# Kernel tuning notes

Hardware: AMD Instinct MI355X
Metric: run time of the kernel (lower is better)

Reference implementation:

```python
import jax, jax.numpy as jnp
import numpy as np

N, E, R = 50000, 500000, 3
IN, HID, OUT = 128, 128, 128
NEG_SLOPE = 0.2


def setup_inputs() -> dict:
    key = jax.random.key(0)
    ks = jax.random.split(key, 16)
    g = lambda i, shape: jax.random.normal(ks[i], shape, jnp.float32) * 0.1
    return {
        "x": jax.random.normal(ks[0], (N, IN), jnp.float32),
        "edge_index": jax.random.randint(ks[1], (2, E), 0, N, jnp.int32),
        "edge_type": jax.random.randint(ks[2], (E,), 0, R, jnp.int32),
        "edge_attr": jax.random.normal(ks[3], (E, 1), jnp.float32),
        # conv1 params (RGATConv: per-relation weight, q/k/e attention vectors, edge lin, bias)
        "w1": g(4, (R, IN, HID)), "q1": g(5, (HID, 1)), "k1": g(6, (HID, 1)),
        "le1": g(7, (1, HID)), "e1": g(8, (HID, 1)), "b1": jnp.zeros((HID,), jnp.float32),
        # conv2 params
        "w2": g(9, (R, HID, OUT)), "q2": g(10, (OUT, 1)), "k2": g(11, (OUT, 1)),
        "le2": g(12, (1, OUT)), "e2": g(13, (OUT, 1)), "b2": jnp.zeros((OUT,), jnp.float32),
    }


def _rgat_conv(x, src, dst, edge_type, edge_attr, w, q, k, le, e, b):
    """PyG RGATConv: heads=1, dim=1, additive-self-attention, across-relation softmax."""
    n = x.shape[0]
    # Per-relation linear at node level (equiv. to per-edge bmm with w[edge_type])
    xw = jnp.einsum('ni,rio->rno', x, w)            # [R, N, C]
    x_j = xw[edge_type, src]                          # [E, C] transformed source feats
    x_i = xw[edge_type, dst]                          # [E, C] transformed target feats
    # additive attention logits: q(x_i) + k(x_j) + e(lin_edge(edge_attr))
    alpha = x_i @ q + x_j @ k + (edge_attr @ le) @ e  # [E, 1]
    alpha = jax.nn.leaky_relu(alpha, negative_slope=NEG_SLOPE)
    # across-relation softmax over incoming edges of each target node
    amax = jax.ops.segment_max(alpha, dst, num_segments=n)
    amax = jnp.where(jnp.isfinite(amax), amax, 0.0)   # empty segments -> 0
    ex = jnp.exp(alpha - amax[dst])
    denom = jax.ops.segment_sum(ex, dst, num_segments=n)
    alpha = ex / (denom[dst] + 1e-16)
    # weighted scatter-add aggregation, then bias (concat=True, heads=1)
    out = jax.ops.segment_sum(alpha * x_j, dst, num_segments=n)  # [N, C]
    return out + b


def reference(x, edge_index, edge_type, edge_attr,
              w1, q1, k1, le1, e1, b1,
              w2, q2, k2, le2, e2, b2):
    src, dst = edge_index[0], edge_index[1]
    h = jax.nn.relu(_rgat_conv(x, src, dst, edge_type, edge_attr, w1, q1, k1, le1, e1, b1))
    return _rgat_conv(h, src, dst, edge_type, edge_attr, w2, q2, k2, le2, e2, b2)
```

## Files before the change

### kernel.cpp

```cpp
#include <hip/hip_runtime.h>
#include <hip/hip_bf16.h>
#include <math.h>

typedef __bf16 bf16x8 __attribute__((ext_vector_type(8)));
typedef float f32x4 __attribute__((ext_vector_type(4)));

#define CDIM 128

__global__ void sentinel_kernel(float* outf) {
  if (threadIdx.x == 0) outf[0] = 12345.0f;
}

__global__ __launch_bounds__(256) void prep_kernel(
    const float* __restrict__ w1, const float* __restrict__ w2,
    __hip_bfloat16* __restrict__ wt,
    const float* __restrict__ le1, const float* __restrict__ e1,
    const float* __restrict__ le2, const float* __restrict__ e2,
    float* __restrict__ outc, int* __restrict__ deg, int perW, int n) {
  const int b = blockIdx.x;
  const int tid = threadIdx.x;
  if (b < 48) {
    int t = b * 256 + tid;
    if (t >= perW * 2) return;
    const float* w = (t < perW) ? w1 : w2;
    int tt = (t < perW) ? t : t - perW;
    int r = tt >> 11;
    int rem = tt & 2047;
    int kb = rem >> 7;
    int o = rem & 127;
    const float* wr = w + ((size_t)r << 14);
    union { __hip_bfloat16 h[8]; int4 v; } u;
#pragma unroll
    for (int j = 0; j < 8; ++j)
      u.h[j] = __float2bfloat16(wr[(size_t)(kb * 8 + j) * CDIM + o]);
    *reinterpret_cast<int4*>(wt + (size_t)t * 8) = u.v;
  } else if (b == 48) {
    if (tid < 64) {
      float v1 = le1[tid] * e1[tid] + le1[tid + 64] * e1[tid + 64];
      float v2 = le2[tid] * e2[tid] + le2[tid + 64] * e2[tid + 64];
#pragma unroll
      for (int off = 32; off > 0; off >>= 1) {
        v1 += __shfl_xor(v1, off, 64);
        v2 += __shfl_xor(v2, off, 64);
      }
      if (tid == 0) { outc[0] = v1; outc[1] = v2; }
    }
  } else {
    int i = (b - 49) * 256 + tid;
    if (i < n) deg[i] = 0;
  }
}


__global__ __launch_bounds__(256) void hist_kernel(const int* __restrict__ dstv,
                                                   int* __restrict__ deg, int E) {
  int e = blockIdx.x * 256 + threadIdx.x;
  if (e < E) atomicAdd(&deg[dstv[e]], 1);
}

__global__ __launch_bounds__(256) void scan1_kernel(const int* __restrict__ deg,
                                                    int* __restrict__ rowptr,
                                                    int* __restrict__ partials, int n) {
  __shared__ int sh[256];
  int t = threadIdx.x;
  int base = blockIdx.x * 1024;
  int idx = base + t * 4;
  int v[4]; int s = 0;
#pragma unroll
  for (int j = 0; j < 4; ++j) { v[j] = (idx + j < n) ? deg[idx + j] : 0; s += v[j]; }
  sh[t] = s;
  __syncthreads();
  for (int off = 1; off < 256; off <<= 1) {
    int x = (t >= off) ? sh[t - off] : 0;
    __syncthreads();
    sh[t] += x;
    __syncthreads();
  }
  int excl = sh[t] - s;
  if (t == 255) partials[blockIdx.x] = sh[255];
  int run = excl;
#pragma unroll
  for (int j = 0; j < 4; ++j) {
    if (idx + j < n) rowptr[idx + j] = run;
    run += v[j];
  }
}

__global__ __launch_bounds__(256) void scan3_kernel(int* __restrict__ rowptr,
                                                    int* __restrict__ cursor,
                                                    const int* __restrict__ partials,
                                                    int nb, int n, int E) {
  __shared__ int spfx[64];
  int t = threadIdx.x;
  if (t < 64) {
    int pv = (t < nb) ? partials[t] : 0;
    int v = pv;
#pragma unroll
    for (int off = 1; off < 64; off <<= 1) {
      int u = __shfl_up(v, off, 64);
      if (t >= off) v += u;
    }
    spfx[t] = v - pv;
  }
  __syncthreads();
  int i = blockIdx.x * 256 + t;
  if (i < n) {
    int v = rowptr[i] + spfx[i >> 10];
    rowptr[i] = v;
    cursor[i] = v;
  } else if (i == n) {
    rowptr[n] = E;
  }
}

__global__ __launch_bounds__(256) void scatter_kernel(
    const int* __restrict__ srcv, const int* __restrict__ dstv,
    const int* __restrict__ etype, const float* __restrict__ eattr,
    int* __restrict__ cursor, int2* __restrict__ kattr, int E, int n) {
  int e = blockIdx.x * 256 + threadIdx.x;
  if (e >= E) return;
  int p = atomicAdd(&cursor[dstv[e]], 1);
  kattr[p] = make_int2(etype[e] * n + srcv[e], __float_as_int(eattr[e]));
}

__global__ __launch_bounds__(256) void gemm_xw_kernel(
    const float* __restrict__ xin, const __hip_bfloat16* __restrict__ wt,
    const float* __restrict__ qv, const float* __restrict__ kv,
    __hip_bfloat16* __restrict__ xwout, float* __restrict__ sq, float* __restrict__ sk,
    int n) {
  __shared__ __hip_bfloat16 wlds[16 * 128 * 8];
  __shared__ float qls[128], kls[128];
  const int base = blockIdx.x * 64;
  const int tid = threadIdx.x;
  const int wave = tid >> 6, lane = tid & 63;
  const int quad = lane >> 4, c16 = lane & 15;

  if (tid < 128) qls[tid] = qv[tid];
  else kls[tid - 128] = kv[tid - 128];

  bf16x8 zf;
#pragma unroll
  for (int j = 0; j < 8; ++j) zf[j] = (__bf16)0.0f;

  const int m = base + wave * 16 + c16;
  const bool ok = m < n;
  bf16x8 af[4];
#pragma unroll
  for (int ks = 0; ks < 4; ++ks) {
    if (ok) {
      const float* xp = xin + (size_t)m * CDIM + ks * 32 + quad * 8;
      f32x4 x0 = *reinterpret_cast<const f32x4*>(xp);
      f32x4 x1 = *reinterpret_cast<const f32x4*>(xp + 4);
      bf16x8 a;
#pragma unroll
      for (int j = 0; j < 4; ++j) { a[j] = (__bf16)x0[j]; a[4 + j] = (__bf16)x1[j]; }
      af[ks] = a;
    } else {
      af[ks] = zf;
    }
  }

  for (int r = 0; r < 3; ++r) {
    if (r) __syncthreads();
    {
      const int4* src = reinterpret_cast<const int4*>(wt + ((size_t)r << 14));
      int4* dst = reinterpret_cast<int4*>(wlds);
#pragma unroll
      for (int i = 0; i < 8; ++i) dst[tid + i * 256] = src[tid + i * 256];
    }
    __syncthreads();

    f32x4 acc[8];
#pragma unroll
    for (int ot = 0; ot < 8; ++ot) acc[ot] = (f32x4){0.f, 0.f, 0.f, 0.f};

#pragma unroll
    for (int ks = 0; ks < 4; ++ks) {
#pragma unroll
      for (int ot = 0; ot < 8; ++ot) {
        bf16x8 b = *reinterpret_cast<const bf16x8*>(
            &wlds[(((ks * 4 + quad) * 128) + ot * 16 + c16) * 8]);
        acc[ot] = __builtin_amdgcn_mfma_f32_16x16x32_bf16(b, af[ks], acc[ot], 0, 0, 0);
      }
    }

    __hip_bfloat16* rp = xwout + (((size_t)r * n + m) << 7) + quad * 4;
    float s_q = 0.f, s_k = 0.f;
#pragma unroll
    for (int ot = 0; ot < 8; ++ot) {
      f32x4 a = acc[ot];
      f32x4 q4 = *reinterpret_cast<const f32x4*>(&qls[ot * 16 + quad * 4]);
      f32x4 k4 = *reinterpret_cast<const f32x4*>(&kls[ot * 16 + quad * 4]);
      s_q += a[0] * q4[0] + a[1] * q4[1] + a[2] * q4[2] + a[3] * q4[3];
      s_k += a[0] * k4[0] + a[1] * k4[1] + a[2] * k4[2] + a[3] * k4[3];
      if (ok) {
        union { __hip_bfloat16 b4[4]; uint2 u; } pk;
#pragma unroll
        for (int t = 0; t < 4; ++t) pk.b4[t] = __float2bfloat16(a[t]);
        *reinterpret_cast<uint2*>(rp + ot * 16) = pk.u;
      }
    }
    s_q += __shfl_xor(s_q, 16, 64);
    s_q += __shfl_xor(s_q, 32, 64);
    s_k += __shfl_xor(s_k, 16, 64);
    s_k += __shfl_xor(s_k, 32, 64);
    if (quad == 0 && ok) {
      sq[(size_t)r * n + m] = s_q;
      sk[(size_t)r * n + m] = s_k;
    }
  }
}

__global__ __launch_bounds__(256) void aggregate_kernel(
    const int* __restrict__ rowptr, const int2* __restrict__ kattr,
    const float* __restrict__ sq, const float* __restrict__ sk,
    const __hip_bfloat16* __restrict__ xw, const float* __restrict__ bias,
    const float* __restrict__ cscal, float* __restrict__ out, int n, int do_relu) {
  const int wave = threadIdx.x >> 6, lane = threadIdx.x & 63;
  const int node = blockIdx.x * 4 + wave;
  if (node >= n) return;
  const int g = lane >> 4;
  const int sub = lane & 15;
  const float c = cscal[0];
  const int n2 = n * 2;

  const int start = rowptr[node];
  const int deg = rowptr[node + 1] - start;
  const float s0 = sq[node], s1 = sq[n + node], s2 = sq[n2 + node];

  float acc[8];
#pragma unroll
  for (int t = 0; t < 8; ++t) acc[t] = 0.f;
  float den = 0.f;

  for (int j0 = 0; j0 < deg; j0 += 16) {
    const int jb = j0 + (g << 2);
    int2 ka[4];
#pragma unroll
    for (int t = 0; t < 4; ++t) {
      int idx = jb + t;
      ka[t] = kattr[start + (idx < deg ? idx : 0)];
    }
    float w[4];
    bf16x8 f[4];
#pragma unroll
    for (int t = 0; t < 4; ++t) {
      int kk = ka[t].x;
      float sv = (kk >= n2) ? s2 : ((kk >= n) ? s1 : s0);
      float l = sv + sk[kk] + c * __int_as_float(ka[t].y);
      l = l > 0.f ? l : 0.2f * l;
      w[t] = (jb + t < deg) ? __expf(l) : 0.f;
      f[t] = *reinterpret_cast<const bf16x8*>(xw + ((size_t)kk << 7) + sub * 8);
    }
#pragma unroll
    for (int t = 0; t < 8; ++t)
      acc[t] += w[0] * (float)f[0][t] + w[1] * (float)f[1][t] +
                w[2] * (float)f[2][t] + w[3] * (float)f[3][t];
    den += (w[0] + w[1]) + (w[2] + w[3]);
  }

#pragma unroll
  for (int t = 0; t < 8; ++t) {
    acc[t] += __shfl_xor(acc[t], 16, 64);
    acc[t] += __shfl_xor(acc[t], 32, 64);
  }
  den += __shfl_xor(den, 16, 64);
  den += __shfl_xor(den, 32, 64);

  if (g == 0) {
    float inv = 1.0f / (den + 1e-16f);
    f32x4 b0 = *reinterpret_cast<const f32x4*>(bias + sub * 8);
    f32x4 b1 = *reinterpret_cast<const f32x4*>(bias + sub * 8 + 4);
    f32x4 o0, o1;
#pragma unroll
    for (int t = 0; t < 4; ++t) {
      o0[t] = acc[t] * inv + b0[t];
      o1[t] = acc[4 + t] * inv + b1[t];
    }
    if (do_relu) {
#pragma unroll
      for (int t = 0; t < 4; ++t) {
        o0[t] = fmaxf(o0[t], 0.f);
        o1[t] = fmaxf(o1[t], 0.f);
      }
    }
    float* op = out + (size_t)node * CDIM + sub * 8;
    *reinterpret_cast<f32x4*>(op) = o0;
    *reinterpret_cast<f32x4*>(op + 4) = o1;
  }
}


extern "C" void kernel_launch(void* const* d_in, const int* in_sizes, int n_in,
                              void* d_out, int out_size, void* d_ws, size_t ws_size,
                              hipStream_t stream) {
  const float* x     = (const float*)d_in[0];
  const int*   eidx  = (const int*)d_in[1];
  const int*   etype = (const int*)d_in[2];
  const float* eattr = (const float*)d_in[3];
  const float* w1  = (const float*)d_in[4];
  const float* q1  = (const float*)d_in[5];
  const float* k1  = (const float*)d_in[6];
  const float* le1 = (const float*)d_in[7];
  const float* e1  = (const float*)d_in[8];
  const float* b1  = (const float*)d_in[9];
  const float* w2  = (const float*)d_in[10];
  const float* q2  = (const float*)d_in[11];
  const float* k2  = (const float*)d_in[12];
  const float* le2 = (const float*)d_in[13];
  const float* e2  = (const float*)d_in[14];
  const float* b2  = (const float*)d_in[15];

  const int N = in_sizes[0] / CDIM;
  const int E = in_sizes[2];
  const int R = in_sizes[4] / (CDIM * CDIM);
  const int* srcv = eidx;
  const int* dstv = eidx + E;

  char* p = (char*)d_ws;
  auto alloc = [&](size_t bytes) -> void* {
    void* q = (void*)p;
    p += (bytes + 255) & ~(size_t)255;
    return q;
  };
  float* sq       = (float*)alloc((size_t)R * N * 4);
  float* sk       = (float*)alloc((size_t)R * N * 4);
  int*   deg      = (int*)alloc((size_t)N * 4);
  int*   rowptr   = (int*)alloc((size_t)(N + 1) * 4);
  int*   cursor   = (int*)alloc((size_t)N * 4);
  int*   partials = (int*)alloc(4096);
  int2*  kattr    = (int2*)alloc((size_t)E * 8);
  __hip_bfloat16* wt = (__hip_bfloat16*)alloc((size_t)2 * R * CDIM * CDIM * 2);
  float* cscal    = (float*)alloc(256);
  __hip_bfloat16* xw = (__hip_bfloat16*)alloc((size_t)R * N * CDIM * 2);

  size_t needed = (size_t)(p - (char*)d_ws);
  if (needed > ws_size) {
    sentinel_kernel<<<1, 64, 0, stream>>>((float*)d_out);
    return;
  }

  float* outp = (float*)d_out;
  float* hbuf = outp;

  const int eg = (E + 255) / 256;
  const int nb = (N + 1023) / 1024;
  const int nodes4 = (N + 3) / 4;
  const int perW = R * 2048;
  const int prep_grid = 49 + (N + 255) / 256;

  prep_kernel<<<prep_grid, 256, 0, stream>>>(w1, w2, wt, le1, e1, le2, e2,
                                             cscal, deg, perW, N);

  hist_kernel<<<eg, 256, 0, stream>>>(dstv, deg, E);
  scan1_kernel<<<nb, 256, 0, stream>>>(deg, rowptr, partials, N);
  scan3_kernel<<<(N + 1 + 255) / 256, 256, 0, stream>>>(rowptr, cursor, partials, nb, N, E);
  scatter_kernel<<<eg, 256, 0, stream>>>(srcv, dstv, etype, eattr, cursor, kattr, E, N);

  dim3 ggrid((N + 63) / 64);

  gemm_xw_kernel<<<ggrid, 256, 0, stream>>>(x, wt, q1, k1, xw, sq, sk, N);
  aggregate_kernel<<<nodes4, 256, 0, stream>>>(rowptr, kattr, sq, sk, xw, b1,
                                               cscal + 0, hbuf, N, 1);

  gemm_xw_kernel<<<ggrid, 256, 0, stream>>>(hbuf, wt + (size_t)R * CDIM * CDIM,
                                            q2, k2, xw, sq, sk, N);
  aggregate_kernel<<<nodes4, 256, 0, stream>>>(rowptr, kattr, sq, sk, xw, b2,
                                               cscal + 1, outp, N, 0);
}
```

Before: 270.5 us.

## Fuse prep with histogram and gemm with scatter, widen gemm tiles, node-per-quarter-wave aggregation

Folds the degree histogram into the weight-prep kernel and replaces the in-kernel degree zeroing with a memset. Runs the layer-1 GEMM and the CSR edge scatter as one launch, split by block index. Each GEMM block now covers 128 rows (two 16-row subtiles per wave), so every LDS weight fragment feeds two MFMAs. Aggregation maps one node to each 16-lane group instead of one node per wave, which drops the cross-group shuffle reduction but serialises each node's edges within a single group and may cause load imbalance on high-degree nodes.

New measurement: 241.4 us. 10.8% less time.

```diff
diff --git a/kernel.cpp b/kernel.cpp
--- a/kernel.cpp
+++ b/kernel.cpp
@@ -11,12 +11,13 @@
   if (threadIdx.x == 0) outf[0] = 12345.0f;
 }
 
-__global__ __launch_bounds__(256) void prep_kernel(
+__global__ __launch_bounds__(256) void prep_hist_kernel(
     const float* __restrict__ w1, const float* __restrict__ w2,
     __hip_bfloat16* __restrict__ wt,
     const float* __restrict__ le1, const float* __restrict__ e1,
     const float* __restrict__ le2, const float* __restrict__ e2,
-    float* __restrict__ outc, int* __restrict__ deg, int perW, int n) {
+    float* __restrict__ outc, const int* __restrict__ dstv,
+    int* __restrict__ deg, int perW, int E) {
   const int b = blockIdx.x;
   const int tid = threadIdx.x;
   if (b < 48) {
@@ -46,17 +47,11 @@
       if (tid == 0) { outc[0] = v1; outc[1] = v2; }
     }
   } else {
-    int i = (b - 49) * 256 + tid;
-    if (i < n) deg[i] = 0;
-  }
-}
-
-
-__global__ __launch_bounds__(256) void hist_kernel(const int* __restrict__ dstv,
-                                                   int* __restrict__ deg, int E) {
-  int e = blockIdx.x * 256 + threadIdx.x;
-  if (e < E) atomicAdd(&deg[dstv[e]], 1);
-}
+    int e = (b - 49) * 256 + tid;
+    if (e < E) atomicAdd(&deg[dstv[e]], 1);
+  }
+}
+
 
 __global__ __launch_bounds__(256) void scan1_kernel(const int* __restrict__ deg,
                                                     int* __restrict__ rowptr,
@@ -113,14 +108,122 @@
   }
 }
 
-__global__ __launch_bounds__(256) void scatter_kernel(
+__device__ __forceinline__ void gemm_body(
+    int tileb, const float* __restrict__ xin, const __hip_bfloat16* __restrict__ wt,
+    const float* __restrict__ qv, const float* __restrict__ kv,
+    __hip_bfloat16* __restrict__ xwout, float* __restrict__ sq,
+    float* __restrict__ sk, int n, __hip_bfloat16* wlds, float* qls, float* kls) {
+  const int base = tileb * 128;
+  const int tid = threadIdx.x;
+  const int wave = tid >> 6, lane = tid & 63;
+  const int quad = lane >> 4, c16 = lane & 15;
+
+  if (tid < 128) qls[tid] = qv[tid];
+  else kls[tid - 128] = kv[tid - 128];
+
+  bf16x8 zf;
+#pragma unroll
+  for (int j = 0; j < 8; ++j) zf[j] = (__bf16)0.0f;
+
+  bf16x8 af[2][4];
+#pragma unroll
+  for (int h = 0; h < 2; ++h) {
+    int m = base + wave * 32 + h * 16 + c16;
+#pragma unroll
+    for (int ks = 0; ks < 4; ++ks) {
+      if (m < n) {
+        const float* xp = xin + (size_t)m * CDIM + ks * 32 + quad * 8;
+        f32x4 x0 = *reinterpret_cast<const f32x4*>(xp);
+        f32x4 x1 = *reinterpret_cast<const f32x4*>(xp + 4);
+        bf16x8 a;
+#pragma unroll
+        for (int j = 0; j < 4; ++j) { a[j] = (__bf16)x0[j]; a[4 + j] = (__bf16)x1[j]; }
+        af[h][ks] = a;
+      } else {
+        af[h][ks] = zf;
+      }
+    }
+  }
+
+  for (int r = 0; r < 3; ++r) {
+    if (r) __syncthreads();
+    {
+      const int4* src = reinterpret_cast<const int4*>(wt + ((size_t)r << 14));
+      int4* dst = reinterpret_cast<int4*>(wlds);
+#pragma unroll
+      for (int i = 0; i < 8; ++i) dst[tid + i * 256] = src[tid + i * 256];
+    }
+    __syncthreads();
+
+    f32x4 acc[2][8];
+#pragma unroll
+    for (int h = 0; h < 2; ++h)
+#pragma unroll
+      for (int ot = 0; ot < 8; ++ot) acc[h][ot] = (f32x4){0.f, 0.f, 0.f, 0.f};
+
+#pragma unroll
+    for (int ks = 0; ks < 4; ++ks) {
+#pragma unroll
+      for (int ot = 0; ot < 8; ++ot) {
+        bf16x8 b = *reinterpret_cast<const bf16x8*>(
+            &wlds[(((ks * 4 + quad) * 128) + ot * 16 + c16) * 8]);
+        acc[0][ot] = __builtin_amdgcn_mfma_f32_16x16x32_bf16(b, af[0][ks], acc[0][ot], 0, 0, 0);
+        acc[1][ot] = __builtin_amdgcn_mfma_f32_16x16x32_bf16(b, af[1][ks], acc[1][ot], 0, 0, 0);
+      }
+    }
+
+#pragma unroll
+    for (int h = 0; h < 2; ++h) {
+      const int grow = base + wave * 32 + h * 16 + c16;
+      const bool ok = grow < n;
+      __hip_bfloat16* rp = xwout + (((size_t)r * n + grow) << 7) + quad * 4;
+      float s_q = 0.f, s_k = 0.f;
+#pragma unroll
+      for (int ot = 0; ot < 8; ++ot) {
+        f32x4 a = acc[h][ot];
+        f32x4 q4 = *reinterpret_cast<const f32x4*>(&qls[ot * 16 + quad * 4]);
+        f32x4 k4 = *reinterpret_cast<const f32x4*>(&kls[ot * 16 + quad * 4]);
+        s_q += a[0] * q4[0] + a[1] * q4[1] + a[2] * q4[2] + a[3] * q4[3];
+        s_k += a[0] * k4[0] + a[1] * k4[1] + a[2] * k4[2] + a[3] * k4[3];
+        if (ok) {
+          union { __hip_bfloat16 b4[4]; uint2 u; } pk;
+#pragma unroll
+          for (int t = 0; t < 4; ++t) pk.b4[t] = __float2bfloat16(a[t]);
+          *reinterpret_cast<uint2*>(rp + ot * 16) = pk.u;
+        }
+      }
+      s_q += __shfl_xor(s_q, 16, 64);
+      s_q += __shfl_xor(s_q, 32, 64);
+      s_k += __shfl_xor(s_k, 16, 64);
+      s_k += __shfl_xor(s_k, 32, 64);
+      if (quad == 0 && ok) {
+        sq[(size_t)r * n + grow] = s_q;
+        sk[(size_t)r * n + grow] = s_k;
+      }
+    }
+  }
+}
+
+__global__ __launch_bounds__(256) void gemm_scatter_kernel(
+    const float* __restrict__ xin, const __hip_bfloat16* __restrict__ wt,
+    const float* __restrict__ qv, const float* __restrict__ kv,
+    __hip_bfloat16* __restrict__ xwout, float* __restrict__ sq, float* __restrict__ sk,
     const int* __restrict__ srcv, const int* __restrict__ dstv,
     const int* __restrict__ etype, const float* __restrict__ eattr,
-    int* __restrict__ cursor, int2* __restrict__ kattr, int E, int n) {
-  int e = blockIdx.x * 256 + threadIdx.x;
-  if (e >= E) return;
-  int p = atomicAdd(&cursor[dstv[e]], 1);
-  kattr[p] = make_int2(etype[e] * n + srcv[e], __float_as_int(eattr[e]));
+    int* __restrict__ cursor, int2* __restrict__ kattr,
+    int NT, int n, int E) {
+  __shared__ __hip_bfloat16 wlds[16 * 128 * 8];
+  __shared__ float qls[128], kls[128];
+  const int b = blockIdx.x;
+  if (b < NT) {
+    gemm_body(b, xin, wt, qv, kv, xwout, sq, sk, n, wlds, qls, kls);
+  } else {
+    int e = (b - NT) * 256 + threadIdx.x;
+    if (e < E) {
+      int p = atomicAdd(&cursor[dstv[e]], 1);
+      kattr[p] = make_int2(etype[e] * n + srcv[e], __float_as_int(eattr[e]));
+    }
+  }
 }
 
 __global__ __launch_bounds__(256) void gemm_xw_kernel(
@@ -130,85 +233,7 @@
     int n) {
   __shared__ __hip_bfloat16 wlds[16 * 128 * 8];
   __shared__ float qls[128], kls[128];
-  const int base = blockIdx.x * 64;
-  const int tid = threadIdx.x;
-  const int wave = tid >> 6, lane = tid & 63;
-  const int quad = lane >> 4, c16 = lane & 15;
-
-  if (tid < 128) qls[tid] = qv[tid];
-  else kls[tid - 128] = kv[tid - 128];
-
-  bf16x8 zf;
-#pragma unroll
-  for (int j = 0; j < 8; ++j) zf[j] = (__bf16)0.0f;
-
-  const int m = base + wave * 16 + c16;
-  const bool ok = m < n;
-  bf16x8 af[4];
-#pragma unroll
-  for (int ks = 0; ks < 4; ++ks) {
-    if (ok) {
-      const float* xp = xin + (size_t)m * CDIM + ks * 32 + quad * 8;
-      f32x4 x0 = *reinterpret_cast<const f32x4*>(xp);
-      f32x4 x1 = *reinterpret_cast<const f32x4*>(xp + 4);
-      bf16x8 a;
-#pragma unroll
-      for (int j = 0; j < 4; ++j) { a[j] = (__bf16)x0[j]; a[4 + j] = (__bf16)x1[j]; }
-      af[ks] = a;
-    } else {
-      af[ks] = zf;
-    }
-  }
-
-  for (int r = 0; r < 3; ++r) {
-    if (r) __syncthreads();
-    {
-      const int4* src = reinterpret_cast<const int4*>(wt + ((size_t)r << 14));
-      int4* dst = reinterpret_cast<int4*>(wlds);
-#pragma unroll
-      for (int i = 0; i < 8; ++i) dst[tid + i * 256] = src[tid + i * 256];
-    }
-    __syncthreads();
-
-    f32x4 acc[8];
-#pragma unroll
-    for (int ot = 0; ot < 8; ++ot) acc[ot] = (f32x4){0.f, 0.f, 0.f, 0.f};
-
-#pragma unroll
-    for (int ks = 0; ks < 4; ++ks) {
-#pragma unroll
-      for (int ot = 0; ot < 8; ++ot) {
-        bf16x8 b = *reinterpret_cast<const bf16x8*>(
-            &wlds[(((ks * 4 + quad) * 128) + ot * 16 + c16) * 8]);
-        acc[ot] = __builtin_amdgcn_mfma_f32_16x16x32_bf16(b, af[ks], acc[ot], 0, 0, 0);
-      }
-    }
-
-    __hip_bfloat16* rp = xwout + (((size_t)r * n + m) << 7) + quad * 4;
-    float s_q = 0.f, s_k = 0.f;
-#pragma unroll
-    for (int ot = 0; ot < 8; ++ot) {
-      f32x4 a = acc[ot];
-      f32x4 q4 = *reinterpret_cast<const f32x4*>(&qls[ot * 16 + quad * 4]);
-      f32x4 k4 = *reinterpret_cast<const f32x4*>(&kls[ot * 16 + quad * 4]);
-      s_q += a[0] * q4[0] + a[1] * q4[1] + a[2] * q4[2] + a[3] * q4[3];
-      s_k += a[0] * k4[0] + a[1] * k4[1] + a[2] * k4[2] + a[3] * k4[3];
-      if (ok) {
-        union { __hip_bfloat16 b4[4]; uint2 u; } pk;
-#pragma unroll
-        for (int t = 0; t < 4; ++t) pk.b4[t] = __float2bfloat16(a[t]);
-        *reinterpret_cast<uint2*>(rp + ot * 16) = pk.u;
-      }
-    }
-    s_q += __shfl_xor(s_q, 16, 64);
-    s_q += __shfl_xor(s_q, 32, 64);
-    s_k += __shfl_xor(s_k, 16, 64);
-    s_k += __shfl_xor(s_k, 32, 64);
-    if (quad == 0 && ok) {
-      sq[(size_t)r * n + m] = s_q;
-      sk[(size_t)r * n + m] = s_k;
-    }
-  }
+  gemm_body(blockIdx.x, xin, wt, qv, kv, xwout, sq, sk, n, wlds, qls, kls);
 }
 
 __global__ __launch_bounds__(256) void aggregate_kernel(
@@ -217,10 +242,10 @@
     const __hip_bfloat16* __restrict__ xw, const float* __restrict__ bias,
     const float* __restrict__ cscal, float* __restrict__ out, int n, int do_relu) {
   const int wave = threadIdx.x >> 6, lane = threadIdx.x & 63;
-  const int node = blockIdx.x * 4 + wave;
-  if (node >= n) return;
   const int g = lane >> 4;
   const int sub = lane & 15;
+  const int node = blockIdx.x * 16 + wave * 4 + g;
+  if (node >= n) return;
   const float c = cscal[0];
   const int n2 = n * 2;
 
@@ -233,12 +258,11 @@
   for (int t = 0; t < 8; ++t) acc[t] = 0.f;
   float den = 0.f;
 
-  for (int j0 = 0; j0 < deg; j0 += 16) {
-    const int jb = j0 + (g << 2);
+  for (int j0 = 0; j0 < deg; j0 += 4) {
     int2 ka[4];
 #pragma unroll
     for (int t = 0; t < 4; ++t) {
-      int idx = jb + t;
+      int idx = j0 + t;
       ka[t] = kattr[start + (idx < deg ? idx : 0)];
     }
     float w[4];
@@ -249,7 +273,7 @@
       float sv = (kk >= n2) ? s2 : ((kk >= n) ? s1 : s0);
       float l = sv + sk[kk] + c * __int_as_float(ka[t].y);
       l = l > 0.f ? l : 0.2f * l;
-      w[t] = (jb + t < deg) ? __expf(l) : 0.f;
+      w[t] = (j0 + t < deg) ? __expf(l) : 0.f;
       f[t] = *reinterpret_cast<const bf16x8*>(xw + ((size_t)kk << 7) + sub * 8);
     }
 #pragma unroll
@@ -259,35 +283,25 @@
     den += (w[0] + w[1]) + (w[2] + w[3]);
   }
 
-#pragma unroll
-  for (int t = 0; t < 8; ++t) {
-    acc[t] += __shfl_xor(acc[t], 16, 64);
-    acc[t] += __shfl_xor(acc[t], 32, 64);
-  }
-  den += __shfl_xor(den, 16, 64);
-  den += __shfl_xor(den, 32, 64);
-
-  if (g == 0) {
-    float inv = 1.0f / (den + 1e-16f);
-    f32x4 b0 = *reinterpret_cast<const f32x4*>(bias + sub * 8);
-    f32x4 b1 = *reinterpret_cast<const f32x4*>(bias + sub * 8 + 4);
-    f32x4 o0, o1;
+  float inv = 1.0f / (den + 1e-16f);
+  f32x4 b0 = *reinterpret_cast<const f32x4*>(bias + sub * 8);
+  f32x4 b1 = *reinterpret_cast<const f32x4*>(bias + sub * 8 + 4);
+  f32x4 o0, o1;
+#pragma unroll
+  for (int t = 0; t < 4; ++t) {
+    o0[t] = acc[t] * inv + b0[t];
+    o1[t] = acc[4 + t] * inv + b1[t];
+  }
+  if (do_relu) {
 #pragma unroll
     for (int t = 0; t < 4; ++t) {
-      o0[t] = acc[t] * inv + b0[t];
-      o1[t] = acc[4 + t] * inv + b1[t];
-    }
-    if (do_relu) {
-#pragma unroll
-      for (int t = 0; t < 4; ++t) {
-        o0[t] = fmaxf(o0[t], 0.f);
-        o1[t] = fmaxf(o1[t], 0.f);
-      }
-    }
-    float* op = out + (size_t)node * CDIM + sub * 8;
-    *reinterpret_cast<f32x4*>(op) = o0;
-    *reinterpret_cast<f32x4*>(op + 4) = o1;
-  }
+      o0[t] = fmaxf(o0[t], 0.f);
+      o1[t] = fmaxf(o1[t], 0.f);
+    }
+  }
+  float* op = out + (size_t)node * CDIM + sub * 8;
+  *reinterpret_cast<f32x4*>(op) = o0;
+  *reinterpret_cast<f32x4*>(op + 4) = o1;
 }
 
 
@@ -345,26 +359,28 @@
 
   const int eg = (E + 255) / 256;
   const int nb = (N + 1023) / 1024;
-  const int nodes4 = (N + 3) / 4;
+  const int NT = (N + 127) / 128;
+  const int nodes16 = (N + 15) / 16;
   const int perW = R * 2048;
-  const int prep_grid = 49 + (N + 255) / 256;
-
-  prep_kernel<<<prep_grid, 256, 0, stream>>>(w1, w2, wt, le1, e1, le2, e2,
-                                             cscal, deg, perW, N);
-
-  hist_kernel<<<eg, 256, 0, stream>>>(dstv, deg, E);
+
+  hipMemsetAsync(deg, 0, (size_t)N * 4, stream);
+
+  prep_hist_kernel<<<49 + eg, 256, 0, stream>>>(w1, w2, wt, le1, e1, le2, e2,
+                                                cscal, dstv, deg, perW, E);
+
   scan1_kernel<<<nb, 256, 0, stream>>>(deg, rowptr, partials, N);
   scan3_kernel<<<(N + 1 + 255) / 256, 256, 0, stream>>>(rowptr, cursor, partials, nb, N, E);
-  scatter_kernel<<<eg, 256, 0, stream>>>(srcv, dstv, etype, eattr, cursor, kattr, E, N);
-
-  dim3 ggrid((N + 63) / 64);
-
-  gemm_xw_kernel<<<ggrid, 256, 0, stream>>>(x, wt, q1, k1, xw, sq, sk, N);
-  aggregate_kernel<<<nodes4, 256, 0, stream>>>(rowptr, kattr, sq, sk, xw, b1,
-                                               cscal + 0, hbuf, N, 1);
-
-  gemm_xw_kernel<<<ggrid, 256, 0, stream>>>(hbuf, wt + (size_t)R * CDIM * CDIM,
-                                            q2, k2, xw, sq, sk, N);
-  aggregate_kernel<<<nodes4, 256, 0, stream>>>(rowptr, kattr, sq, sk, xw, b2,
-                                               cscal + 1, outp, N, 0);
-}
+
+  gemm_scatter_kernel<<<NT + eg, 256, 0, stream>>>(x, wt, q1, k1, xw, sq, sk,
+                                                   srcv, dstv, etype, eattr,
+                                                   cursor, kattr, NT, N, E);
+
+  aggregate_kernel<<<nodes16, 256, 0, stream>>>(rowptr, kattr, sq, sk, xw, b1,
+                                                cscal + 0, hbuf, N, 1);
+
+  gemm_xw_kernel<<<NT, 256, 0, stream>>>(hbuf, wt + (size_t)R * CDIM * CDIM,
+                                         q2, k2, xw, sq, sk, N);
+
+  aggregate_kernel<<<nodes16, 256, 0, stream>>>(rowptr, kattr, sq, sk, xw, b2,
+                                                cscal + 1, outp, N, 0);
+}
```
